# Optimization experiments

Measured on AMD Instinct MI355X. Metric: run time of the kernel, lower is better.

Reference implementation:

```python
import jax, jax.numpy as jnp
import numpy as np

# dims
N = 50000      # total nodes in merged batch graph
M = 250000     # edges for GNN propagation
E = 200000     # candidate edges scored by mixture-Bernoulli head
MAXN = 512     # max_num_nodes (padded adjacency row length)
H = 128        # hidden_dim = embedding_dim = msg_dim
EF = 128       # edge_feat_dim = 2 * att_edge_dim
ATT = 128      # att_hidden_dim
K = 20         # num_mix_component
L = 3          # num_GNN_layers
S = 512        # num_subgraph
B = 16         # batch of graphs
C = 1          # num_canonical_order


def setup_inputs() -> dict:
    key = jax.random.key(0)
    ks = list(jax.random.split(key, 64))
    it = iter(ks)
    nk = lambda: next(it)
    d = {}
    d['node_feat'] = jax.random.normal(nk(), (N, MAXN), jnp.float32)
    d['edge'] = jax.random.randint(nk(), (M, 2), 0, N, dtype=jnp.int32)
    d['edge_feat'] = jax.random.normal(nk(), (M, EF), jnp.float32)
    d['node_idx_gnn'] = jax.random.randint(nk(), (E, 2), 0, N, dtype=jnp.int32)
    d['label'] = (jax.random.uniform(nk(), (E,)) < 0.1).astype(jnp.float32)
    # even sorted partition of E candidate edges into S subgraphs (all nonempty)
    d['subgraph_idx'] = ((jnp.arange(E) * S) // E).astype(jnp.int32)
    # bc_idx = repeat_interleave(arange(B*C), subgraphs_per_graph)
    d['bc_idx'] = jnp.repeat(jnp.arange(B * C, dtype=jnp.int32), S // (B * C))
    # params
    def lin(k, out_d, in_d):
        return jax.random.normal(k, (out_d, in_d), jnp.float32) * (1.0 / np.sqrt(in_d))
    d['dec_W'] = lin(nk(), H, MAXN); d['dec_b'] = jnp.zeros((H,), jnp.float32)
    d['msg_W1'] = jnp.stack([lin(nk(), H, H + EF) for _ in range(L)])
    d['msg_b1'] = jnp.zeros((L, H), jnp.float32)
    d['msg_W2'] = jnp.stack([lin(nk(), H, H) for _ in range(L)])
    d['msg_b2'] = jnp.zeros((L, H), jnp.float32)
    d['att_W1'] = jnp.stack([lin(nk(), ATT, H + EF) for _ in range(L)])
    d['att_b1'] = jnp.zeros((L, ATT), jnp.float32)
    d['att_W2'] = jnp.stack([lin(nk(), H, ATT) for _ in range(L)])
    d['att_b2'] = jnp.zeros((L, H), jnp.float32)
    d['gru_Wih'] = jnp.stack([lin(nk(), 3 * H, H) for _ in range(L)])
    d['gru_bih'] = jnp.zeros((L, 3 * H), jnp.float32)
    d['gru_Whh'] = jnp.stack([lin(nk(), 3 * H, H) for _ in range(L)])
    d['gru_bhh'] = jnp.zeros((L, 3 * H), jnp.float32)
    d['th_W1'] = lin(nk(), H, H); d['th_b1'] = jnp.zeros((H,), jnp.float32)
    d['th_W2'] = lin(nk(), H, H); d['th_b2'] = jnp.zeros((H,), jnp.float32)
    d['th_W3'] = lin(nk(), K, H); d['th_b3'] = jnp.zeros((K,), jnp.float32)
    d['al_W1'] = lin(nk(), H, H); d['al_b1'] = jnp.zeros((H,), jnp.float32)
    d['al_W2'] = lin(nk(), H, H); d['al_b2'] = jnp.zeros((H,), jnp.float32)
    d['al_W3'] = lin(nk(), K, H); d['al_b3'] = jnp.zeros((K,), jnp.float32)
    return d


def _gran_forward(node_feat, edge_feat, label, dec_W, dec_b, msg_W1, msg_b1,
                  msg_W2, msg_b2, att_W1, att_b1, att_W2, att_b2, gru_Wih,
                  gru_bih, gru_Whh, gru_bhh, th_W1, th_b1, th_W2, th_b2,
                  th_W3, th_b3, al_W1, al_b1, al_W2, al_b2, al_W3, al_b3,
                  edge, node_idx_gnn, subgraph_idx, bc_idx):
    n = node_feat.shape[0]
    # decoder_input: Linear(max_num_nodes -> embedding_dim)
    state = node_feat @ dec_W.T + dec_b  # [N, H]
    src, dst = edge[:, 0], edge[:, 1]
    for l in range(L):
        if l > 0:
            state = jax.nn.relu(state)
        # _prop: gather diff, msg MLP, sigmoid attention gate, scatter-sum, GRU
        diff = state[src] - state[dst]                       # [M, H]
        ei = jnp.concatenate([diff, edge_feat], axis=1)      # [M, H+EF]
        msg = jax.nn.relu(ei @ msg_W1[l].T + msg_b1[l]) @ msg_W2[l].T + msg_b2[l]
        att = jax.nn.sigmoid(jax.nn.relu(ei @ att_W1[l].T + att_b1[l]) @ att_W2[l].T + att_b2[l])
        agg = jax.ops.segment_sum(msg * att, dst, num_segments=n)  # [N, H]
        # torch GRUCell
        gi = agg @ gru_Wih[l].T + gru_bih[l]
        gh = state @ gru_Whh[l].T + gru_bhh[l]
        i_r, i_z, i_n = jnp.split(gi, 3, axis=-1)
        h_r, h_z, h_n = jnp.split(gh, 3, axis=-1)
        r = jax.nn.sigmoid(i_r + h_r)
        z = jax.nn.sigmoid(i_z + h_z)
        nn_ = jnp.tanh(i_n + r * h_n)
        state = (1.0 - z) * nn_ + z * state
    # mixture-Bernoulli heads on candidate-edge node-state diffs
    d2 = state[node_idx_gnn[:, 0]] - state[node_idx_gnn[:, 1]]  # [E, H]
    def mlp3(x, W1, b1, W2, b2, W3, b3):
        h = jax.nn.relu(x @ W1.T + b1)
        h = jax.nn.relu(h @ W2.T + b2)
        return h @ W3.T + b3
    log_theta = mlp3(d2, th_W1, th_b1, th_W2, th_b2, th_W3, th_b3)  # [E, K]
    log_alpha = mlp3(d2, al_W1, al_b1, al_W2, al_b2, al_W3, al_b3)  # [E, K]
    # mixture_bernoulli_loss (pos_weight = 1.0)
    y = label[:, None]
    adj_loss = jax.nn.softplus(-log_theta) + (1.0 - y) * log_theta  # BCEWithLogits, [E, K]
    const = jax.ops.segment_sum(jnp.ones((label.shape[0],), log_theta.dtype), subgraph_idx, num_segments=S)
    reduce_adj = jax.ops.segment_sum(adj_loss, subgraph_idx, num_segments=S)     # [S, K]
    reduce_la = jax.ops.segment_sum(log_alpha, subgraph_idx, num_segments=S)
    reduce_la = jax.nn.log_softmax(reduce_la / const[:, None], axis=-1)
    log_prob = jax.scipy.special.logsumexp(-reduce_adj + reduce_la, axis=1)      # [S]
    bc_log_prob = jax.ops.segment_sum(log_prob, bc_idx, num_segments=B * C)
    bc_const = jax.ops.segment_sum(const, bc_idx, num_segments=B * C)
    bc_loss = (bc_log_prob / bc_const).reshape(B, C)
    b_loss = jax.scipy.special.logsumexp(bc_loss, axis=1)  # logsumexp over orderings
    return jnp.mean(-b_loss)


def reference(node_feat, edge, edge_feat, node_idx_gnn, label, subgraph_idx,
              bc_idx, dec_W, dec_b, msg_W1, msg_b1, msg_W2, msg_b2, att_W1,
              att_b1, att_W2, att_b2, gru_Wih, gru_bih, gru_Whh, gru_bhh,
              th_W1, th_b1, th_W2, th_b2, th_W3, th_b3, al_W1, al_b1, al_W2,
              al_b2, al_W3, al_b3):
    return _gran_forward(node_feat, edge_feat, label, dec_W, dec_b, msg_W1,
                         msg_b1, msg_W2, msg_b2, att_W1, att_b1, att_W2,
                         att_b2, gru_Wih, gru_bih, gru_Whh, gru_bhh, th_W1,
                         th_b1, th_W2, th_b2, th_W3, th_b3, al_W1, al_b1,
                         al_W2, al_b2, al_W3, al_b3, edge, node_idx_gnn,
                         subgraph_idx, bc_idx)
```

## Files before the change

kernel.cpp:

```cpp
#include <hip/hip_runtime.h>
#include <cstdint>
#include <cstddef>


typedef __bf16 bf16x8 __attribute__((ext_vector_type(8)));
typedef short  s16x8  __attribute__((ext_vector_type(8)));
typedef short  s16x4  __attribute__((ext_vector_type(4)));
typedef float  f32x4  __attribute__((ext_vector_type(4)));

__device__ inline unsigned short f2bf(float f) {
    return __builtin_bit_cast(unsigned short, (__bf16)f);
}
__device__ inline float bf2f(unsigned short b) {
    return __uint_as_float(((unsigned int)b) << 16);
}
__device__ inline unsigned int pk2(float a, float b) {
    return ((unsigned int)f2bf(b) << 16) | f2bf(a);
}
__device__ inline f32x4 MFMA(bf16x8 a, bf16x8 b, f32x4 c) {
    return __builtin_amdgcn_mfma_f32_16x16x32_bf16(a, b, c, 0, 0, 0);
}

__device__ inline bf16x8 ld_swz(const char* lds, int row, int unit) {
    return *(const bf16x8*)(lds + row * 256 + ((unit ^ (row & 7)) << 4));
}
__device__ inline void hid_write(char* HID, int h0, int erow, s16x4 s4) {
    int unit = h0 >> 3;
    *(s16x4*)(HID + erow * 256 + ((unit ^ (erow & 7)) << 4) + ((h0 & 4) << 1)) = s4;
}
__device__ inline s16x4 ld_swz4(const char* lds, int row, int c0) {
    int unit = c0 >> 3;
    return *(const s16x4*)(lds + row * 256 + ((unit ^ (row & 7)) << 4) + ((c0 & 4) << 1));
}
__device__ inline bf16x8 ldA(const short* __restrict__ Wb, int K, int row, int koff) {
    return *(const bf16x8*)(Wb + (size_t)row * K + koff);
}
__device__ inline bf16x8 ld_f32_frag(const float* __restrict__ p) {
    float4 a = *(const float4*)p, b = *(const float4*)(p + 4);
    s16x8 s;
    s[0] = f2bf(a.x); s[1] = f2bf(a.y); s[2] = f2bf(a.z); s[3] = f2bf(a.w);
    s[4] = f2bf(b.x); s[5] = f2bf(b.y); s[6] = f2bf(b.z); s[7] = f2bf(b.w);
    return __builtin_bit_cast(bf16x8, s);
}

#define NPACK 31
struct PrepackArgs {
    const float* src[NPACK];
    short*       dst[NPACK];
    int stride[NPACK];
    int rows[NPACK];
    int rowsTot[NPACK];
    int cols[NPACK];
};

__global__ void prepack(PrepackArgs a) {
    int e = blockIdx.y;
    int row = blockIdx.x;
    if (row >= a.rowsTot[e]) return;
    int c8 = threadIdx.x;
    if (c8 * 8 >= a.cols[e]) return;
    s16x8 s = {};
    if (row < a.rows[e]) {
        const float* p = a.src[e] + (size_t)row * a.stride[e] + c8 * 8;
        float4 x = *(const float4*)p, y = *(const float4*)(p + 4);
        s[0] = f2bf(x.x); s[1] = f2bf(x.y); s[2] = f2bf(x.z); s[3] = f2bf(x.w);
        s[4] = f2bf(y.x); s[5] = f2bf(y.y); s[6] = f2bf(y.z); s[7] = f2bf(y.w);
    }
    *(s16x8*)(a.dst[e] + (size_t)row * a.cols[e] + c8 * 8) = s;
}

__device__ inline void proj_gemm_store(const char* ST, char* PJ,
                                       const short* __restrict__ projW,
                                       short* __restrict__ proj,
                                       int rb, int R, int tid)
{
    const int l = tid & 63, w = tid >> 6;
    f32x4 accP[2][2][4] = {};
#pragma unroll
    for (int ks = 0; ks < 4; ++ks) {
        int koff = ks * 32 + (l >> 4) * 8;
        bf16x8 aw[2][2];
#pragma unroll
        for (int pc = 0; pc < 2; ++pc)
#pragma unroll
            for (int mt = 0; mt < 2; ++mt)
                aw[pc][mt] = ldA(projW, 128, pc * 128 + 32 * w + 16 * mt + (l & 15), koff);
#pragma unroll
        for (int n = 0; n < 4; ++n) {
            bf16x8 b = ld_swz(ST, 16 * n + (l & 15), ks * 4 + (l >> 4));
#pragma unroll
            for (int pc = 0; pc < 2; ++pc)
#pragma unroll
                for (int mt = 0; mt < 2; ++mt)
                    accP[pc][mt][n] = MFMA(aw[pc][mt], b, accP[pc][mt][n]);
        }
    }
    const int half = w >> 1;
#pragma unroll
    for (int hh = 0; hh < 2; ++hh) {
        __syncthreads();
        if (half == hh) {
#pragma unroll
            for (int pc = 0; pc < 2; ++pc)
#pragma unroll
                for (int mt = 0; mt < 2; ++mt) {
                    int h0 = 32 * w + 16 * mt + ((l >> 4) << 2);
                    int colp = 2 * h0 + 4 * pc - 128 * hh;
#pragma unroll
                    for (int n = 0; n < 4; ++n) {
                        f32x4 v = accP[pc][mt][n];
                        s16x4 s4;
                        s4[0] = f2bf(v[0]); s4[1] = f2bf(v[1]);
                        s4[2] = f2bf(v[2]); s4[3] = f2bf(v[3]);
                        hid_write(PJ, colp, 16 * n + (l & 15), s4);
                    }
                }
        }
        __syncthreads();
#pragma unroll
        for (int p2 = 0; p2 < 4; ++p2) {
            int row = p2 * 16 + (tid >> 4);
            int r = rb + row;
            if (r < R) {
                bf16x8 v = ld_swz(PJ, row, tid & 15);
                *(s16x8*)(proj + (size_t)r * 256 + hh * 128 + (tid & 15) * 8) =
                    __builtin_bit_cast(s16x8, v);
            }
        }
    }
}

__global__ __launch_bounds__(256, 3)
void dec_proj(const float* __restrict__ nf, int R,
              const short* __restrict__ decWb, const float* __restrict__ bias,
              const short* __restrict__ projW,
              short* __restrict__ sOut, short* __restrict__ proj)
{
    __shared__ char ST[16384];
    __shared__ char PJ[16384];
    const int tid = threadIdx.x, l = tid & 63, w = tid >> 6;
    const int rb = blockIdx.x * 64;

    const float* brow[4];
#pragma unroll
    for (int n = 0; n < 4; ++n) {
        int row = rb + 16 * n + (l & 15); if (row >= R) row = R - 1;
        brow[n] = nf + (size_t)row * 512;
    }

    f32x4 acc[2][4] = {};
    for (int kc = 0; kc < 512; kc += 128) {
#pragma unroll
        for (int ks = 0; ks < 4; ++ks) {
            int koff = kc + ks * 32 + (l >> 4) * 8;
            bf16x8 a0 = ldA(decWb, 512, 32 * w + (l & 15), koff);
            bf16x8 a1 = ldA(decWb, 512, 32 * w + 16 + (l & 15), koff);
#pragma unroll
            for (int n = 0; n < 4; ++n) {
                bf16x8 b = ld_f32_frag(brow[n] + koff);
                acc[0][n] = MFMA(a0, b, acc[0][n]);
                acc[1][n] = MFMA(a1, b, acc[1][n]);
            }
        }
    }
#pragma unroll
    for (int mt = 0; mt < 2; ++mt) {
        int c0 = 32 * w + 16 * mt + ((l >> 4) << 2);
        float4 bv = *(const float4*)&bias[c0];
#pragma unroll
        for (int n = 0; n < 4; ++n) {
            f32x4 v = acc[mt][n];
            s16x4 s4;
            s4[0] = f2bf(v[0] + bv.x); s4[1] = f2bf(v[1] + bv.y);
            s4[2] = f2bf(v[2] + bv.z); s4[3] = f2bf(v[3] + bv.w);
            hid_write(ST, c0, 16 * n + (l & 15), s4);
        }
    }
    __syncthreads();
#pragma unroll
    for (int p2 = 0; p2 < 4; ++p2) {
        int row = p2 * 16 + (tid >> 4);
        int r = rb + row;
        if (r < R) {
            bf16x8 v = ld_swz(ST, row, tid & 15);
            *(s16x8*)(sOut + (size_t)r * 128 + (tid & 15) * 8) =
                __builtin_bit_cast(s16x8, v);
        }
    }
    proj_gemm_store(ST, PJ, projW, proj, rb, R, tid);
}

template<int HAS_PROJ>
__global__ __launch_bounds__(256, 3)
void node_fused6(const short* __restrict__ msgatt, const int* __restrict__ rowptr,
                 const short* __restrict__ sin_,
                 const short* __restrict__ Wih, const short* __restrict__ Whh,
                 const float* __restrict__ bih, const float* __restrict__ bhh,
                 const short* __restrict__ projW,
                 short* __restrict__ sOut, short* __restrict__ proj, int R)
{
    __shared__ char AGT[16384];
    __shared__ char SIN[16384];
    __shared__ char ST[16384];
    const int tid = threadIdx.x, l = tid & 63, w = tid >> 6;
    const int rb = blockIdx.x * 64;

#pragma unroll 1
    for (int pass = 0; pass < 4; ++pass) {
        int row = pass * 16 + (tid >> 4);
        int node = rb + row;
        int u = tid & 15;
        float acc[8] = {};
        s16x8 sv = {};
        if (node < R) {
            int b = rowptr[node], e = rowptr[node + 1];
            for (int i = b; i < e; ++i) {
                s16x8 x = *(const s16x8*)(msgatt + (size_t)i * 128 + u * 8);
#pragma unroll
                for (int j = 0; j < 8; ++j) acc[j] += bf2f((unsigned short)x[j]);
            }
            sv = *(const s16x8*)(sin_ + (size_t)node * 128 + u * 8);
        }
        s16x8 o;
#pragma unroll
        for (int j = 0; j < 8; ++j) o[j] = f2bf(acc[j]);
        *(s16x8*)(AGT + row * 256 + ((u ^ (row & 7)) << 4)) = o;
        *(s16x8*)(SIN + row * 256 + ((u ^ (row & 7)) << 4)) = sv;
    }
    __syncthreads();

#pragma unroll 1
    for (int nh = 0; nh < 2; ++nh) {
        unsigned int rpk[2][2][2], zpk[2][2][2];
#pragma unroll 1
        for (int p = 0; p < 3; ++p) {
            f32x4 gia[2][2] = {}, gha[2][2] = {};
#pragma unroll
            for (int ks = 0; ks < 4; ++ks) {
                int koff = ks * 32 + (l >> 4) * 8;
                bf16x8 ai0 = ldA(Wih, 128, p * 128 + 32 * w + (l & 15), koff);
                bf16x8 ai1 = ldA(Wih, 128, p * 128 + 32 * w + 16 + (l & 15), koff);
                bf16x8 ah0 = ldA(Whh, 128, p * 128 + 32 * w + (l & 15), koff);
                bf16x8 ah1 = ldA(Whh, 128, p * 128 + 32 * w + 16 + (l & 15), koff);
#pragma unroll
                for (int n = 0; n < 2; ++n) {
                    int row = 32 * nh + 16 * n + (l & 15);
                    bf16x8 ba = ld_swz(AGT, row, ks * 4 + (l >> 4));
                    bf16x8 bs = ld_swz(SIN, row, ks * 4 + (l >> 4));
                    gia[0][n] = MFMA(ai0, ba, gia[0][n]);
                    gia[1][n] = MFMA(ai1, ba, gia[1][n]);
                    gha[0][n] = MFMA(ah0, bs, gha[0][n]);
                    gha[1][n] = MFMA(ah1, bs, gha[1][n]);
                }
            }
#pragma unroll
            for (int mt = 0; mt < 2; ++mt) {
                int c0 = 32 * w + 16 * mt + ((l >> 4) << 2);
                float4 bi = *(const float4*)&bih[p * 128 + c0];
                float4 bh = *(const float4*)&bhh[p * 128 + c0];
                float biv[4] = {bi.x, bi.y, bi.z, bi.w};
                float bhv[4] = {bh.x, bh.y, bh.z, bh.w};
#pragma unroll
                for (int n = 0; n < 2; ++n) {
                    int row = 32 * nh + 16 * n + (l & 15);
                    float gv[4], hv[4];
#pragma unroll
                    for (int q = 0; q < 4; ++q) {
                        gv[q] = gia[mt][n][q] + biv[q];
                        hv[q] = gha[mt][n][q] + bhv[q];
                    }
                    if (p == 0) {
                        rpk[mt][n][0] = pk2(1.f / (1.f + expf(-(gv[0] + hv[0]))),
                                            1.f / (1.f + expf(-(gv[1] + hv[1]))));
                        rpk[mt][n][1] = pk2(1.f / (1.f + expf(-(gv[2] + hv[2]))),
                                            1.f / (1.f + expf(-(gv[3] + hv[3]))));
                    } else if (p == 1) {
                        zpk[mt][n][0] = pk2(1.f / (1.f + expf(-(gv[0] + hv[0]))),
                                            1.f / (1.f + expf(-(gv[1] + hv[1]))));
                        zpk[mt][n][1] = pk2(1.f / (1.f + expf(-(gv[2] + hv[2]))),
                                            1.f / (1.f + expf(-(gv[3] + hv[3]))));
                    } else {
                        s16x4 sv = ld_swz4(SIN, row, c0);
                        s16x4 s4;
#pragma unroll
                        for (int q = 0; q < 4; ++q) {
                            unsigned int ru = rpk[mt][n][q >> 1], zu = zpk[mt][n][q >> 1];
                            float r = bf2f((unsigned short)((q & 1) ? (ru >> 16) : (ru & 0xffffu)));
                            float z = bf2f((unsigned short)((q & 1) ? (zu >> 16) : (zu & 0xffffu)));
                            float nn = tanhf(gv[q] + r * hv[q]);
                            float o = (1.f - z) * nn + z * bf2f((unsigned short)sv[q]);
                            s4[q] = f2bf(HAS_PROJ ? fmaxf(o, 0.f) : o);
                        }
                        hid_write(ST, c0, row, s4);
                    }
                }
            }
        }
    }
    __syncthreads();
#pragma unroll
    for (int p2 = 0; p2 < 4; ++p2) {
        int row = p2 * 16 + (tid >> 4);
        int r = rb + row;
        if (r < R) {
            bf16x8 v = ld_swz(ST, row, tid & 15);
            *(s16x8*)(sOut + (size_t)r * 128 + (tid & 15) * 8) =
                __builtin_bit_cast(s16x8, v);
        }
    }
    if (HAS_PROJ)
        proj_gemm_store(ST, AGT, projW, proj, rb, R, tid);
}

__global__ __launch_bounds__(256, 3)
void edge_fused2(const short* __restrict__ efc,
                 const int* __restrict__ srcs, const int* __restrict__ dsts,
                 const short* __restrict__ proj,
                 const short* __restrict__ mW1b, const short* __restrict__ mW2,
                 const short* __restrict__ aW1b, const short* __restrict__ aW2,
                 const float* __restrict__ mb1, const float* __restrict__ mb2,
                 const float* __restrict__ ab1, const float* __restrict__ ab2,
                 short* __restrict__ msgatt, int M, int ntiles)
{
    __shared__ char HIDm[16384];
    __shared__ char HIDa[16384];
    const int tid = threadIdx.x, l = tid & 63, w = tid >> 6;
    int q = ntiles >> 3, r = ntiles & 7;
    int xcd = blockIdx.x & 7, o = blockIdx.x >> 3;
    int tile = (xcd < r ? xcd * (q + 1) : r * (q + 1) + (xcd - r) * q) + o;
    const int pb = tile * 64;

    const char* erow[4];
    int dstv[4];
    s16x8 psv[2][4];
    {
#pragma unroll
        for (int n = 0; n < 4; ++n) {
            int pos = pb + 16 * n + (l & 15); if (pos >= M) pos = M - 1;
            int sv = srcs[pos];
            dstv[n] = dsts[pos];
            erow[n] = (const char*)(efc + (size_t)pos * 128);
#pragma unroll
            for (int mt = 0; mt < 2; ++mt) {
                int off = 2 * (32 * w + 16 * mt + ((l >> 4) << 2));
                psv[mt][n] = *(const s16x8*)(proj + (size_t)sv * 256 + off);
            }
        }
    }

    f32x4 accm[2][4] = {}, acca[2][4] = {};
#pragma unroll
    for (int ks = 0; ks < 4; ++ks) {
        int koff = ks * 32 + (l >> 4) * 8;
        bf16x8 am0 = ldA(mW1b, 128, 32 * w + (l & 15), koff);
        bf16x8 am1 = ldA(mW1b, 128, 32 * w + 16 + (l & 15), koff);
        bf16x8 aa0 = ldA(aW1b, 128, 32 * w + (l & 15), koff);
        bf16x8 aa1 = ldA(aW1b, 128, 32 * w + 16 + (l & 15), koff);
#pragma unroll
        for (int n = 0; n < 4; ++n) {
            bf16x8 b = *(const bf16x8*)(erow[n] + koff * 2);
            accm[0][n] = MFMA(am0, b, accm[0][n]);
            accm[1][n] = MFMA(am1, b, accm[1][n]);
            acca[0][n] = MFMA(aa0, b, acca[0][n]);
            acca[1][n] = MFMA(aa1, b, acca[1][n]);
        }
    }
#pragma unroll
    for (int mt = 0; mt < 2; ++mt) {
        int h0 = 32 * w + 16 * mt + ((l >> 4) << 2);
        float4 bm = *(const float4*)&mb1[h0];
        float4 ba = *(const float4*)&ab1[h0];
        float bmv[4] = {bm.x, bm.y, bm.z, bm.w};
        float bav[4] = {ba.x, ba.y, ba.z, ba.w};
#pragma unroll
        for (int n = 0; n < 4; ++n) {
            s16x8 ps = psv[mt][n];
            s16x8 pd = *(const s16x8*)(proj + (size_t)dstv[n] * 256 + 2 * h0);
            f32x4 vm = accm[mt][n], va = acca[mt][n];
            s16x4 sm, sa;
#pragma unroll
            for (int qq = 0; qq < 4; ++qq) {
                float m_ = vm[qq] + bmv[qq] + bf2f((unsigned short)ps[qq])
                           - bf2f((unsigned short)pd[qq]);
                float a_ = va[qq] + bav[qq] + bf2f((unsigned short)ps[qq + 4])
                           - bf2f((unsigned short)pd[qq + 4]);
                sm[qq] = f2bf(fmaxf(m_, 0.f));
                sa[qq] = f2bf(fmaxf(a_, 0.f));
            }
            hid_write(HIDm, h0, 16 * n + (l & 15), sm);
            hid_write(HIDa, h0, 16 * n + (l & 15), sa);
        }
    }
    __syncthreads();

    f32x4 acc2m[2][4] = {}, acc2a[2][4] = {};
#pragma unroll
    for (int ks = 0; ks < 4; ++ks) {
        int koff = ks * 32 + (l >> 4) * 8;
        bf16x8 wm0 = ldA(mW2, 128, 32 * w + (l & 15), koff);
        bf16x8 wm1 = ldA(mW2, 128, 32 * w + 16 + (l & 15), koff);
        bf16x8 wa0 = ldA(aW2, 128, 32 * w + (l & 15), koff);
        bf16x8 wa1 = ldA(aW2, 128, 32 * w + 16 + (l & 15), koff);
#pragma unroll
        for (int n = 0; n < 4; ++n) {
            bf16x8 bm = ld_swz(HIDm, 16 * n + (l & 15), ks * 4 + (l >> 4));
            bf16x8 ba = ld_swz(HIDa, 16 * n + (l & 15), ks * 4 + (l >> 4));
            acc2m[0][n] = MFMA(wm0, bm, acc2m[0][n]);
            acc2m[1][n] = MFMA(wm1, bm, acc2m[1][n]);
            acc2a[0][n] = MFMA(wa0, ba, acc2a[0][n]);
            acc2a[1][n] = MFMA(wa1, ba, acc2a[1][n]);
        }
    }
    __syncthreads();
#pragma unroll
    for (int mt = 0; mt < 2; ++mt) {
        int c0 = 32 * w + 16 * mt + ((l >> 4) << 2);
        float4 bm2 = *(const float4*)&mb2[c0];
        float4 ba2 = *(const float4*)&ab2[c0];
#pragma unroll
        for (int n = 0; n < 4; ++n) {
            f32x4 m_ = acc2m[mt][n], a_ = acc2a[mt][n];
            float o0 = (m_[0] + bm2.x) / (1.f + expf(-(a_[0] + ba2.x)));
            float o1 = (m_[1] + bm2.y) / (1.f + expf(-(a_[1] + ba2.y)));
            float o2 = (m_[2] + bm2.z) / (1.f + expf(-(a_[2] + ba2.z)));
            float o3 = (m_[3] + bm2.w) / (1.f + expf(-(a_[3] + ba2.w)));
            s16x4 s4;
            s4[0] = f2bf(o0); s4[1] = f2bf(o1); s4[2] = f2bf(o2); s4[3] = f2bf(o3);
            hid_write(HIDm, c0, 16 * n + (l & 15), s4);
        }
    }
    __syncthreads();
#pragma unroll
    for (int p2 = 0; p2 < 4; ++p2) {
        int row = p2 * 16 + (tid >> 4);
        int pos = pb + row;
        if (pos < M) {
            bf16x8 v = ld_swz(HIDm, row, tid & 15);
            *(s16x8*)(msgatt + (size_t)pos * 128 + (tid & 15) * 8) =
                __builtin_bit_cast(s16x8, v);
        }
    }
}

__global__ __launch_bounds__(256, 4)
void mlp_loss(const short* __restrict__ sP, const int* __restrict__ gidx,
              const float* __restrict__ label, const int* __restrict__ sg,
              const short* __restrict__ thW1, const short* __restrict__ thW2,
              const short* __restrict__ thW3,
              const float* __restrict__ thb1, const float* __restrict__ thb2,
              const float* __restrict__ thb3,
              const short* __restrict__ alW1, const short* __restrict__ alW2,
              const short* __restrict__ alW3,
              const float* __restrict__ alb1, const float* __restrict__ alb2,
              const float* __restrict__ alb3,
              float* __restrict__ radj, float* __restrict__ rla,
              float* __restrict__ cntS, int E, int S)
{
    __shared__ char D2T[16384];
    __shared__ char HID[16384];
    __shared__ float sacc[2][2][20];
    __shared__ float scnt[2];
    __shared__ int sbase;
    const int tid = threadIdx.x, l = tid & 63, w = tid >> 6;
    const int eb = blockIdx.x * 64;

    if (tid == 0) sbase = sg[eb];
    if (tid < 80) sacc[tid / 40][(tid / 20) & 1][tid % 20] = 0.f;

    if (w == 0) {
        int e = eb + l;
        bool valid = e < E;
        int lsv = valid ? sg[e] - sg[eb] : -1;
        unsigned long long m0 = __ballot(lsv == 0);
        unsigned long long m1 = __ballot(lsv == 1);
        if (l == 0) { scnt[0] = (float)__popcll(m0); scnt[1] = (float)__popcll(m1); }
    }

    for (int i = tid; i < 64 * 16; i += 256) {
        int row = i >> 4, u = i & 15;
        int e = eb + row; if (e >= E) e = E - 1;
        int2 ab = *(const int2*)&gidx[2 * (size_t)e];
        s16x8 x = *(const s16x8*)(sP + (size_t)ab.x * 128 + u * 8);
        s16x8 y = *(const s16x8*)(sP + (size_t)ab.y * 128 + u * 8);
        s16x8 d;
#pragma unroll
        for (int j = 0; j < 8; ++j)
            d[j] = f2bf(bf2f((unsigned short)x[j]) - bf2f((unsigned short)y[j]));
        *(s16x8*)(D2T + row * 256 + ((u ^ (row & 7)) << 4)) = d;
    }
    __syncthreads();

#pragma unroll 1
    for (int pass = 0; pass < 2; ++pass) {
        const short* W1 = pass ? alW1 : thW1;
        const short* W2 = pass ? alW2 : thW2;
        const short* W3 = pass ? alW3 : thW3;
        const float* b1 = pass ? alb1 : thb1;
        const float* b2 = pass ? alb2 : thb2;
        const float* b3 = pass ? alb3 : thb3;

        f32x4 acc[2][4] = {};
#pragma unroll
        for (int ks = 0; ks < 4; ++ks) {
            int koff = ks * 32 + (l >> 4) * 8;
            bf16x8 a0 = ldA(W1, 128, 32 * w + (l & 15), koff);
            bf16x8 a1 = ldA(W1, 128, 32 * w + 16 + (l & 15), koff);
#pragma unroll
            for (int n = 0; n < 4; ++n) {
                bf16x8 b = ld_swz(D2T, 16 * n + (l & 15), ks * 4 + (l >> 4));
                acc[0][n] = MFMA(a0, b, acc[0][n]);
                acc[1][n] = MFMA(a1, b, acc[1][n]);
            }
        }
        __syncthreads();
#pragma unroll
        for (int mt = 0; mt < 2; ++mt) {
            int h0 = 32 * w + 16 * mt + ((l >> 4) << 2);
            float4 bv = *(const float4*)&b1[h0];
#pragma unroll
            for (int n = 0; n < 4; ++n) {
                f32x4 v = acc[mt][n];
                s16x4 s4;
                s4[0] = f2bf(fmaxf(v[0] + bv.x, 0.f));
                s4[1] = f2bf(fmaxf(v[1] + bv.y, 0.f));
                s4[2] = f2bf(fmaxf(v[2] + bv.z, 0.f));
                s4[3] = f2bf(fmaxf(v[3] + bv.w, 0.f));
                hid_write(HID, h0, 16 * n + (l & 15), s4);
            }
        }
        __syncthreads();
        f32x4 acc2[2][4] = {};
#pragma unroll
        for (int ks = 0; ks < 4; ++ks) {
            int koff = ks * 32 + (l >> 4) * 8;
            bf16x8 a0 = ldA(W2, 128, 32 * w + (l & 15), koff);
            bf16x8 a1 = ldA(W2, 128, 32 * w + 16 + (l & 15), koff);
#pragma unroll
            for (int n = 0; n < 4; ++n) {
                bf16x8 b = ld_swz(HID, 16 * n + (l & 15), ks * 4 + (l >> 4));
                acc2[0][n] = MFMA(a0, b, acc2[0][n]);
                acc2[1][n] = MFMA(a1, b, acc2[1][n]);
            }
        }
        __syncthreads();
#pragma unroll
        for (int mt = 0; mt < 2; ++mt) {
            int h0 = 32 * w + 16 * mt + ((l >> 4) << 2);
            float4 bv = *(const float4*)&b2[h0];
#pragma unroll
            for (int n = 0; n < 4; ++n) {
                f32x4 v = acc2[mt][n];
                s16x4 s4;
                s4[0] = f2bf(fmaxf(v[0] + bv.x, 0.f));
                s4[1] = f2bf(fmaxf(v[1] + bv.y, 0.f));
                s4[2] = f2bf(fmaxf(v[2] + bv.z, 0.f));
                s4[3] = f2bf(fmaxf(v[3] + bv.w, 0.f));
                hid_write(HID, h0, 16 * n + (l & 15), s4);
            }
        }
        __syncthreads();
        f32x4 acc3[2] = {};
#pragma unroll
        for (int ks = 0; ks < 4; ++ks) {
            int koff = ks * 32 + (l >> 4) * 8;
            bf16x8 a0 = ldA(W3, 128, (l & 15), koff);
            bf16x8 a1 = ldA(W3, 128, 16 + (l & 15), koff);
            bf16x8 b = ld_swz(HID, 16 * w + (l & 15), ks * 4 + (l >> 4));
            acc3[0] = MFMA(a0, b, acc3[0]);
            acc3[1] = MFMA(a1, b, acc3[1]);
        }
        {
            int e = eb + 16 * w + (l & 15);
            bool val = e < E;
            float lsf = val ? (float)(sg[e] - sbase) : 0.f;
            float yv = (pass == 0 && val) ? label[e] : 0.f;
#pragma unroll
            for (int mt = 0; mt < 2; ++mt) {
#pragma unroll
                for (int qq = 0; qq < 4; ++qq) {
                    int k = 16 * mt + ((l >> 4) << 2) + qq;
                    bool kok = k < 20;
                    float bk = kok ? b3[k] : 0.f;
                    float vv = 0.f;
                    if (val && kok) {
                        float t = acc3[mt][qq] + bk;
                        if (pass == 0) {
                            float sp = fmaxf(-t, 0.f) + log1pf(expf(-fabsf(t)));
                            vv = sp + (1.f - yv) * t;
                        } else {
                            vv = t;
                        }
                    }
                    float vA = vv * (1.f - lsf), vB = vv * lsf;
                    vA += __shfl_xor(vA, 1); vB += __shfl_xor(vB, 1);
                    vA += __shfl_xor(vA, 2); vB += __shfl_xor(vB, 2);
                    vA += __shfl_xor(vA, 4); vB += __shfl_xor(vB, 4);
                    vA += __shfl_xor(vA, 8); vB += __shfl_xor(vB, 8);
                    if ((l & 15) == 0 && kok) {
                        atomicAdd(&sacc[pass][0][k], vA);
                        if (vB != 0.f) atomicAdd(&sacc[pass][1][k], vB);
                    }
                }
            }
        }
    }
    __syncthreads();
    if (tid < 40) {
        int ls = tid / 20, k = tid % 20;
        int s = sbase + ls;
        if (s < S) {
            float v  = sacc[0][ls][k];
            float v2 = sacc[1][ls][k];
            if (v  != 0.f) atomicAdd(&radj[s * 20 + k], v);
            if (v2 != 0.f) atomicAdd(&rla[s * 20 + k], v2);
        }
    }
    if (tid < 2) {
        int s = sbase + tid;
        if (s < S && scnt[tid] != 0.f) atomicAdd(&cntS[s], scnt[tid]);
    }
}

__global__ void csr_count(const int* __restrict__ edge, int* __restrict__ cnt, int M) {
    int e = blockIdx.x * 256 + threadIdx.x;
    if (e < M) atomicAdd(&cnt[edge[2 * (size_t)e + 1]], 1);
}

__global__ void csr_scan(const int* __restrict__ cnt, int* __restrict__ rowptr,
                         int* __restrict__ wofs, int N)
{
    __shared__ int part[1024];
    int t = threadIdx.x;
    int chunk = (N + 1023) / 1024;
    int b0 = t * chunk, b1 = b0 + chunk; if (b1 > N) b1 = N; if (b0 > N) b0 = N;
    int s = 0;
    for (int i = b0; i < b1; ++i) s += cnt[i];
    part[t] = s;
    __syncthreads();
    for (int off = 1; off < 1024; off <<= 1) {
        int v = (t >= off) ? part[t - off] : 0;
        __syncthreads();
        part[t] += v;
        __syncthreads();
    }
    int run = (t ? part[t - 1] : 0);
    for (int i = b0; i < b1; ++i) { rowptr[i] = run; wofs[i] = run; run += cnt[i]; }
    if (t == 1023) rowptr[N] = run;
}

__global__ void csr_scatter2(const int* __restrict__ edge, int* __restrict__ wofs,
                             int* __restrict__ eidx, int* __restrict__ srcs,
                             int* __restrict__ dsts, int M)
{
    int e = blockIdx.x * 256 + threadIdx.x;
    if (e < M) {
        int2 sd = *(const int2*)&edge[2 * (size_t)e];
        int p = atomicAdd(&wofs[sd.y], 1);
        eidx[p] = e; srcs[p] = sd.x; dsts[p] = sd.y;
    }
}

__global__ void ef_gather(const float* __restrict__ ef, const int* __restrict__ eidx,
                          short* __restrict__ efc, int M)
{
    long i = (long)blockIdx.x * 256 + threadIdx.x;
    if (i >= (long)M * 16) return;
    int p = (int)(i >> 4), u = (int)(i & 15);
    int e = eidx[p];
    const float* sp = ef + (size_t)e * 128 + u * 8;
    float4 a = *(const float4*)sp, b = *(const float4*)(sp + 4);
    s16x8 s;
    s[0] = f2bf(a.x); s[1] = f2bf(a.y); s[2] = f2bf(a.z); s[3] = f2bf(a.w);
    s[4] = f2bf(b.x); s[5] = f2bf(b.y); s[6] = f2bf(b.z); s[7] = f2bf(b.w);
    *(s16x8*)(efc + (size_t)p * 128 + u * 8) = s;
}

__global__ void final_kernel(const float* __restrict__ radj, const float* __restrict__ rla,
                             const float* __restrict__ cnt, const int* __restrict__ bc_idx,
                             float* __restrict__ out)
{
    __shared__ float bcl[16], bcc[16];
    const int s = threadIdx.x;
    if (s < 16) { bcl[s] = 0.f; bcc[s] = 0.f; }
    __syncthreads();
    float c = cnt[s];
    float x[20];
    float mx = -1e30f;
#pragma unroll
    for (int k = 0; k < 20; ++k) { x[k] = rla[s * 20 + k] / c; mx = fmaxf(mx, x[k]); }
    float se = 0.f;
#pragma unroll
    for (int k = 0; k < 20; ++k) se += expf(x[k] - mx);
    float lse = mx + logf(se);
    float t[20];
    float m2 = -1e30f;
#pragma unroll
    for (int k = 0; k < 20; ++k) { t[k] = -radj[s * 20 + k] + x[k] - lse; m2 = fmaxf(m2, t[k]); }
    float s2 = 0.f;
#pragma unroll
    for (int k = 0; k < 20; ++k) s2 += expf(t[k] - m2);
    float lp = m2 + logf(s2);
    atomicAdd(&bcl[bc_idx[s]], lp);
    atomicAdd(&bcc[bc_idx[s]], c);
    __syncthreads();
    if (s == 0) {
        float a = 0.f;
        for (int b = 0; b < 16; ++b) a += bcl[b] / bcc[b];
        out[0] = -a / 16.f;
    }
}

extern "C" void kernel_launch(void* const* d_in, const int* in_sizes, int n_in,
                              void* d_out, int out_size, void* d_ws, size_t ws_size,
                              hipStream_t stream)
{
    const float* node_feat = (const float*)d_in[0];
    const int*   edge      = (const int*)  d_in[1];
    const float* edge_feat = (const float*)d_in[2];
    const int*   gnn_idx   = (const int*)  d_in[3];
    const float* label     = (const float*)d_in[4];
    const int*   sg_idx    = (const int*)  d_in[5];
    const int*   bc_idx    = (const int*)  d_in[6];
    const float* dec_W  = (const float*)d_in[7];
    const float* dec_b  = (const float*)d_in[8];
    const float* msg_W1 = (const float*)d_in[9];
    const float* msg_b1 = (const float*)d_in[10];
    const float* msg_W2 = (const float*)d_in[11];
    const float* msg_b2 = (const float*)d_in[12];
    const float* att_W1 = (const float*)d_in[13];
    const float* att_b1 = (const float*)d_in[14];
    const float* att_W2 = (const float*)d_in[15];
    const float* att_b2 = (const float*)d_in[16];
    const float* gru_Wih = (const float*)d_in[17];
    const float* gru_bih = (const float*)d_in[18];
    const float* gru_Whh = (const float*)d_in[19];
    const float* gru_bhh = (const float*)d_in[20];
    const float* th_W1 = (const float*)d_in[21];
    const float* th_b1 = (const float*)d_in[22];
    const float* th_W2 = (const float*)d_in[23];
    const float* th_b2 = (const float*)d_in[24];
    const float* th_W3 = (const float*)d_in[25];
    const float* th_b3 = (const float*)d_in[26];
    const float* al_W1 = (const float*)d_in[27];
    const float* al_b1 = (const float*)d_in[28];
    const float* al_W2 = (const float*)d_in[29];
    const float* al_b2 = (const float*)d_in[30];
    const float* al_W3 = (const float*)d_in[31];
    const float* al_b3 = (const float*)d_in[32];

    const int N = in_sizes[0] / 512;
    const int M = in_sizes[1] / 2;
    const int E = in_sizes[3] / 2;
    const int S = in_sizes[6];

    size_t off = 0;
    auto alloc = [&](size_t bytes) {
        char* p = (char*)d_ws + off;
        off += (bytes + 255) & ~(size_t)255;
        return p;
    };
    short* decWb  = (short*)alloc((size_t)128 * 512 * 2);
    short* projWb = (short*)alloc((size_t)3 * 256 * 128 * 2);
    short* mW1bB  = (short*)alloc((size_t)3 * 128 * 128 * 2);
    short* aW1bB  = (short*)alloc((size_t)3 * 128 * 128 * 2);
    short* mW2B   = (short*)alloc((size_t)3 * 128 * 128 * 2);
    short* aW2B   = (short*)alloc((size_t)3 * 128 * 128 * 2);
    short* gihB   = (short*)alloc((size_t)3 * 384 * 128 * 2);
    short* ghhB   = (short*)alloc((size_t)3 * 384 * 128 * 2);
    short* thW1B  = (short*)alloc((size_t)128 * 128 * 2);
    short* thW2B  = (short*)alloc((size_t)128 * 128 * 2);
    short* thW3B  = (short*)alloc((size_t)32 * 128 * 2);
    short* alW1B  = (short*)alloc((size_t)128 * 128 * 2);
    short* alW2B  = (short*)alloc((size_t)128 * 128 * 2);
    short* alW3B  = (short*)alloc((size_t)32 * 128 * 2);
    short* sA     = (short*)alloc((size_t)N * 128 * 2);
    short* sB     = (short*)alloc((size_t)N * 128 * 2);
    short* sP     = (short*)alloc((size_t)N * 128 * 2);
    short* efc    = (short*)alloc((size_t)M * 128 * 2);
    short* msgatt = (short*)alloc((size_t)M * 128 * 2);
    short* proj   = (short*)alloc((size_t)N * 256 * 2);
    int*   cntN   = (int*)  alloc((size_t)N * 4);
    int*   wofs   = (int*)  alloc((size_t)N * 4);
    int*   rowptr = (int*)  alloc((size_t)(N + 1) * 4);
    int*   eidx   = (int*)  alloc((size_t)M * 4);
    int*   srcs   = (int*)  alloc((size_t)M * 4);
    int*   dsts   = (int*)  alloc((size_t)M * 4);
    float* radj   = (float*)alloc((size_t)S * 20 * 4);
    float* rla    = (float*)alloc((size_t)S * 20 * 4);
    float* cntS   = (float*)alloc((size_t)S * 4);

    PrepackArgs pa;
    int ei = 0;
    auto add = [&](const float* s, short* d, int stride, int rows, int rowsTot, int cols) {
        pa.src[ei] = s; pa.dst[ei] = d; pa.stride[ei] = stride;
        pa.rows[ei] = rows; pa.rowsTot[ei] = rowsTot; pa.cols[ei] = cols; ++ei;
    };
    add(dec_W, decWb, 512, 128, 128, 512);
    for (int l = 0; l < 3; ++l) {
        add(msg_W1 + (size_t)l * 128 * 256,       projWb + (size_t)l * 256 * 128,          256, 128, 128, 128);
        add(att_W1 + (size_t)l * 128 * 256,       projWb + (size_t)l * 256 * 128 + 16384,  256, 128, 128, 128);
        add(msg_W1 + (size_t)l * 128 * 256 + 128, mW1bB + (size_t)l * 16384,               256, 128, 128, 128);
        add(att_W1 + (size_t)l * 128 * 256 + 128, aW1bB + (size_t)l * 16384,               256, 128, 128, 128);
        add(msg_W2 + (size_t)l * 16384,           mW2B + (size_t)l * 16384,                128, 128, 128, 128);
        add(att_W2 + (size_t)l * 16384,           aW2B + (size_t)l * 16384,                128, 128, 128, 128);
        add(gru_Wih + (size_t)l * 49152,          gihB + (size_t)l * 49152,                128, 384, 384, 128);
        add(gru_Whh + (size_t)l * 49152,          ghhB + (size_t)l * 49152,                128, 384, 384, 128);
    }
    add(th_W1, thW1B, 128, 128, 128, 128);
    add(th_W2, thW2B, 128, 128, 128, 128);
    add(th_W3, thW3B, 128, 20, 32, 128);
    add(al_W1, alW1B, 128, 128, 128, 128);
    add(al_W2, alW2B, 128, 128, 128, 128);
    add(al_W3, alW3B, 128, 20, 32, 128);

    const dim3 blk(256);
    const int gN64 = (N + 63) / 64;
    const int gE64 = (E + 63) / 64;
    const int gMt  = (M + 255) / 256;
    const int ntilesM = (M + 63) / 64;

    hipMemsetAsync(radj, 0, (size_t)(S * 20 * 2 + S) * 4, stream);
    hipMemsetAsync(cntN, 0, (size_t)N * 4, stream);

    prepack<<<dim3(384, NPACK), dim3(64), 0, stream>>>(pa);

    csr_count   <<<gMt, blk, 0, stream>>>(edge, cntN, M);
    csr_scan    <<<1, 1024, 0, stream>>>(cntN, rowptr, wofs, N);
    csr_scatter2<<<gMt, blk, 0, stream>>>(edge, wofs, eidx, srcs, dsts, M);
    ef_gather   <<<(int)(((long)M * 16 + 255) / 256), blk, 0, stream>>>(edge_feat, eidx, efc, M);

    dec_proj<<<gN64, blk, 0, stream>>>(node_feat, N, decWb, dec_b, projWb, sA, proj);

    short* bufs[2] = { sA, sB };
    for (int l = 0; l < 3; ++l) {
        short* sin  = bufs[l & 1];
        short* sout = (l == 2) ? sP : bufs[(l + 1) & 1];
        edge_fused2<<<ntilesM, blk, 0, stream>>>(efc, srcs, dsts, proj,
            mW1bB + (size_t)l * 16384, mW2B + (size_t)l * 16384,
            aW1bB + (size_t)l * 16384, aW2B + (size_t)l * 16384,
            msg_b1 + l * 128, msg_b2 + l * 128,
            att_b1 + l * 128, att_b2 + l * 128,
            msgatt, M, ntilesM);
        if (l < 2) {
            node_fused6<1><<<gN64, blk, 0, stream>>>(msgatt, rowptr, sin,
                gihB + (size_t)l * 49152, ghhB + (size_t)l * 49152,
                gru_bih + l * 384, gru_bhh + l * 384,
                projWb + (size_t)(l + 1) * 256 * 128, sout, proj, N);
        } else {
            node_fused6<0><<<gN64, blk, 0, stream>>>(msgatt, rowptr, sin,
                gihB + (size_t)l * 49152, ghhB + (size_t)l * 49152,
                gru_bih + l * 384, gru_bhh + l * 384,
                nullptr, sout, nullptr, N);
        }
    }

    mlp_loss<<<gE64, blk, 0, stream>>>(sP, gnn_idx, label, sg_idx,
        thW1B, thW2B, thW3B, th_b1, th_b2, th_b3,
        alW1B, alW2B, alW3B, al_b1, al_b2, al_b3,
        radj, rla, cntS, E, S);
    final_kernel<<<1, S, 0, stream>>>(radj, rla, cntS, bc_idx, (float*)d_out);
}
```

Measured before the change: 1.063 ms.

## Compute W1 state term per edge from gathered state difference instead of node projections

Removes the per-node projection GEMM and its N×256 bf16 buffer from the decoder and node kernels. The edge kernel instead gathers source and destination state rows (128 wide), forms their difference in shared memory, and multiplies by the first-half W1 weights with MFMA. This halves the per-edge gather bytes and drops the projection stores. In exchange it adds a per-edge GEMM over M edges rather than N nodes, plus an extra shared buffer and barrier, with bf16 rounding of the difference.

```diff
diff --git a/kernel.cpp b/kernel.cpp
--- a/kernel.cpp
+++ b/kernel.cpp
@@ -69,75 +69,12 @@
     *(s16x8*)(a.dst[e] + (size_t)row * a.cols[e] + c8 * 8) = s;
 }
 
-__device__ inline void proj_gemm_store(const char* ST, char* PJ,
-                                       const short* __restrict__ projW,
-                                       short* __restrict__ proj,
-                                       int rb, int R, int tid)
-{
-    const int l = tid & 63, w = tid >> 6;
-    f32x4 accP[2][2][4] = {};
-#pragma unroll
-    for (int ks = 0; ks < 4; ++ks) {
-        int koff = ks * 32 + (l >> 4) * 8;
-        bf16x8 aw[2][2];
-#pragma unroll
-        for (int pc = 0; pc < 2; ++pc)
-#pragma unroll
-            for (int mt = 0; mt < 2; ++mt)
-                aw[pc][mt] = ldA(projW, 128, pc * 128 + 32 * w + 16 * mt + (l & 15), koff);
-#pragma unroll
-        for (int n = 0; n < 4; ++n) {
-            bf16x8 b = ld_swz(ST, 16 * n + (l & 15), ks * 4 + (l >> 4));
-#pragma unroll
-            for (int pc = 0; pc < 2; ++pc)
-#pragma unroll
-                for (int mt = 0; mt < 2; ++mt)
-                    accP[pc][mt][n] = MFMA(aw[pc][mt], b, accP[pc][mt][n]);
-        }
-    }
-    const int half = w >> 1;
-#pragma unroll
-    for (int hh = 0; hh < 2; ++hh) {
-        __syncthreads();
-        if (half == hh) {
-#pragma unroll
-            for (int pc = 0; pc < 2; ++pc)
-#pragma unroll
-                for (int mt = 0; mt < 2; ++mt) {
-                    int h0 = 32 * w + 16 * mt + ((l >> 4) << 2);
-                    int colp = 2 * h0 + 4 * pc - 128 * hh;
-#pragma unroll
-                    for (int n = 0; n < 4; ++n) {
-                        f32x4 v = accP[pc][mt][n];
-                        s16x4 s4;
-                        s4[0] = f2bf(v[0]); s4[1] = f2bf(v[1]);
-                        s4[2] = f2bf(v[2]); s4[3] = f2bf(v[3]);
-                        hid_write(PJ, colp, 16 * n + (l & 15), s4);
-                    }
-                }
-        }
-        __syncthreads();
-#pragma unroll
-        for (int p2 = 0; p2 < 4; ++p2) {
-            int row = p2 * 16 + (tid >> 4);
-            int r = rb + row;
-            if (r < R) {
-                bf16x8 v = ld_swz(PJ, row, tid & 15);
-                *(s16x8*)(proj + (size_t)r * 256 + hh * 128 + (tid & 15) * 8) =
-                    __builtin_bit_cast(s16x8, v);
-            }
-        }
-    }
-}
-
 __global__ __launch_bounds__(256, 3)
-void dec_proj(const float* __restrict__ nf, int R,
-              const short* __restrict__ decWb, const float* __restrict__ bias,
-              const short* __restrict__ projW,
-              short* __restrict__ sOut, short* __restrict__ proj)
+void dec_kernel(const float* __restrict__ nf, int R,
+                const short* __restrict__ decWb, const float* __restrict__ bias,
+                short* __restrict__ sOut)
 {
     __shared__ char ST[16384];
-    __shared__ char PJ[16384];
     const int tid = threadIdx.x, l = tid & 63, w = tid >> 6;
     const int rb = blockIdx.x * 64;
 
@@ -187,17 +124,15 @@
                 __builtin_bit_cast(s16x8, v);
         }
     }
-    proj_gemm_store(ST, PJ, projW, proj, rb, R, tid);
-}
-
-template<int HAS_PROJ>
+}
+
+template<int HAS_RELU>
 __global__ __launch_bounds__(256, 3)
-void node_fused6(const short* __restrict__ msgatt, const int* __restrict__ rowptr,
+void node_fused7(const short* __restrict__ msgatt, const int* __restrict__ rowptr,
                  const short* __restrict__ sin_,
                  const short* __restrict__ Wih, const short* __restrict__ Whh,
                  const float* __restrict__ bih, const float* __restrict__ bhh,
-                 const short* __restrict__ projW,
-                 short* __restrict__ sOut, short* __restrict__ proj, int R)
+                 short* __restrict__ sOut, int R)
 {
     __shared__ char AGT[16384];
     __shared__ char SIN[16384];
@@ -289,7 +224,7 @@
                             float z = bf2f((unsigned short)((q & 1) ? (zu >> 16) : (zu & 0xffffu)));
                             float nn = tanhf(gv[q] + r * hv[q]);
                             float o = (1.f - z) * nn + z * bf2f((unsigned short)sv[q]);
-                            s4[q] = f2bf(HAS_PROJ ? fmaxf(o, 0.f) : o);
+                            s4[q] = f2bf(HAS_RELU ? fmaxf(o, 0.f) : o);
                         }
                         hid_write(ST, c0, row, s4);
                     }
@@ -308,20 +243,21 @@
                 __builtin_bit_cast(s16x8, v);
         }
     }
-    if (HAS_PROJ)
-        proj_gemm_store(ST, AGT, projW, proj, rb, R, tid);
 }
 
 __global__ __launch_bounds__(256, 3)
-void edge_fused2(const short* __restrict__ efc,
+void edge_fused7(const short* __restrict__ efc,
                  const int* __restrict__ srcs, const int* __restrict__ dsts,
-                 const short* __restrict__ proj,
-                 const short* __restrict__ mW1b, const short* __restrict__ mW2,
-                 const short* __restrict__ aW1b, const short* __restrict__ aW2,
+                 const short* __restrict__ state,
+                 const short* __restrict__ mW1a, const short* __restrict__ mW1b,
+                 const short* __restrict__ mW2,
+                 const short* __restrict__ aW1a, const short* __restrict__ aW1b,
+                 const short* __restrict__ aW2,
                  const float* __restrict__ mb1, const float* __restrict__ mb2,
                  const float* __restrict__ ab1, const float* __restrict__ ab2,
                  short* __restrict__ msgatt, int M, int ntiles)
 {
+    __shared__ char DIF[16384];
     __shared__ char HIDm[16384];
     __shared__ char HIDa[16384];
     const int tid = threadIdx.x, l = tid & 63, w = tid >> 6;
@@ -330,25 +266,45 @@
     int tile = (xcd < r ? xcd * (q + 1) : r * (q + 1) + (xcd - r) * q) + o;
     const int pb = tile * 64;
 
+#pragma unroll 1
+    for (int i = tid; i < 64 * 16; i += 256) {
+        int row = i >> 4, u = i & 15;
+        int pos = pb + row; if (pos >= M) pos = M - 1;
+        int sv = srcs[pos], dv = dsts[pos];
+        s16x8 x = *(const s16x8*)(state + (size_t)sv * 128 + u * 8);
+        s16x8 y = *(const s16x8*)(state + (size_t)dv * 128 + u * 8);
+        s16x8 d;
+#pragma unroll
+        for (int j = 0; j < 8; ++j)
+            d[j] = f2bf(bf2f((unsigned short)x[j]) - bf2f((unsigned short)y[j]));
+        *(s16x8*)(DIF + row * 256 + ((u ^ (row & 7)) << 4)) = d;
+    }
+    __syncthreads();
+
     const char* erow[4];
-    int dstv[4];
-    s16x8 psv[2][4];
-    {
+#pragma unroll
+    for (int n = 0; n < 4; ++n) {
+        int pos = pb + 16 * n + (l & 15); if (pos >= M) pos = M - 1;
+        erow[n] = (const char*)(efc + (size_t)pos * 128);
+    }
+
+    f32x4 accm[2][4] = {}, acca[2][4] = {};
+#pragma unroll
+    for (int ks = 0; ks < 4; ++ks) {
+        int koff = ks * 32 + (l >> 4) * 8;
+        bf16x8 am0 = ldA(mW1a, 128, 32 * w + (l & 15), koff);
+        bf16x8 am1 = ldA(mW1a, 128, 32 * w + 16 + (l & 15), koff);
+        bf16x8 aa0 = ldA(aW1a, 128, 32 * w + (l & 15), koff);
+        bf16x8 aa1 = ldA(aW1a, 128, 32 * w + 16 + (l & 15), koff);
 #pragma unroll
         for (int n = 0; n < 4; ++n) {
-            int pos = pb + 16 * n + (l & 15); if (pos >= M) pos = M - 1;
-            int sv = srcs[pos];
-            dstv[n] = dsts[pos];
-            erow[n] = (const char*)(efc + (size_t)pos * 128);
-#pragma unroll
-            for (int mt = 0; mt < 2; ++mt) {
-                int off = 2 * (32 * w + 16 * mt + ((l >> 4) << 2));
-                psv[mt][n] = *(const s16x8*)(proj + (size_t)sv * 256 + off);
-            }
-        }
-    }
-
-    f32x4 accm[2][4] = {}, acca[2][4] = {};
+            bf16x8 b = ld_swz(DIF, 16 * n + (l & 15), ks * 4 + (l >> 4));
+            accm[0][n] = MFMA(am0, b, accm[0][n]);
+            accm[1][n] = MFMA(am1, b, accm[1][n]);
+            acca[0][n] = MFMA(aa0, b, acca[0][n]);
+            acca[1][n] = MFMA(aa1, b, acca[1][n]);
+        }
+    }
 #pragma unroll
     for (int ks = 0; ks < 4; ++ks) {
         int koff = ks * 32 + (l >> 4) * 8;
@@ -374,18 +330,12 @@
         float bav[4] = {ba.x, ba.y, ba.z, ba.w};
 #pragma unroll
         for (int n = 0; n < 4; ++n) {
-            s16x8 ps = psv[mt][n];
-            s16x8 pd = *(const s16x8*)(proj + (size_t)dstv[n] * 256 + 2 * h0);
             f32x4 vm = accm[mt][n], va = acca[mt][n];
             s16x4 sm, sa;
 #pragma unroll
             for (int qq = 0; qq < 4; ++qq) {
-                float m_ = vm[qq] + bmv[qq] + bf2f((unsigned short)ps[qq])
-                           - bf2f((unsigned short)pd[qq]);
-                float a_ = va[qq] + bav[qq] + bf2f((unsigned short)ps[qq + 4])
-                           - bf2f((unsigned short)pd[qq + 4]);
-                sm[qq] = f2bf(fmaxf(m_, 0.f));
-                sa[qq] = f2bf(fmaxf(a_, 0.f));
+                sm[qq] = f2bf(fmaxf(vm[qq] + bmv[qq], 0.f));
+                sa[qq] = f2bf(fmaxf(va[qq] + bav[qq], 0.f));
             }
             hid_write(HIDm, h0, 16 * n + (l & 15), sm);
             hid_write(HIDa, h0, 16 * n + (l & 15), sa);
@@ -760,7 +710,8 @@
         return p;
     };
     short* decWb  = (short*)alloc((size_t)128 * 512 * 2);
-    short* projWb = (short*)alloc((size_t)3 * 256 * 128 * 2);
+    short* mW1aB  = (short*)alloc((size_t)3 * 128 * 128 * 2);
+    short* aW1aB  = (short*)alloc((size_t)3 * 128 * 128 * 2);
     short* mW1bB  = (short*)alloc((size_t)3 * 128 * 128 * 2);
     short* aW1bB  = (short*)alloc((size_t)3 * 128 * 128 * 2);
     short* mW2B   = (short*)alloc((size_t)3 * 128 * 128 * 2);
@@ -778,7 +729,6 @@
     short* sP     = (short*)alloc((size_t)N * 128 * 2);
     short* efc    = (short*)alloc((size_t)M * 128 * 2);
     short* msgatt = (short*)alloc((size_t)M * 128 * 2);
-    short* proj   = (short*)alloc((size_t)N * 256 * 2);
     int*   cntN   = (int*)  alloc((size_t)N * 4);
     int*   wofs   = (int*)  alloc((size_t)N * 4);
     int*   rowptr = (int*)  alloc((size_t)(N + 1) * 4);
@@ -797,14 +747,14 @@
     };
     add(dec_W, decWb, 512, 128, 128, 512);
     for (int l = 0; l < 3; ++l) {
-        add(msg_W1 + (size_t)l * 128 * 256,       projWb + (size_t)l * 256 * 128,          256, 128, 128, 128);
-        add(att_W1 + (size_t)l * 128 * 256,       projWb + (size_t)l * 256 * 128 + 16384,  256, 128, 128, 128);
-        add(msg_W1 + (size_t)l * 128 * 256 + 128, mW1bB + (size_t)l * 16384,               256, 128, 128, 128);
-        add(att_W1 + (size_t)l * 128 * 256 + 128, aW1bB + (size_t)l * 16384,               256, 128, 128, 128);
-        add(msg_W2 + (size_t)l * 16384,           mW2B + (size_t)l * 16384,                128, 128, 128, 128);
-        add(att_W2 + (size_t)l * 16384,           aW2B + (size_t)l * 16384,                128, 128, 128, 128);
-        add(gru_Wih + (size_t)l * 49152,          gihB + (size_t)l * 49152,                128, 384, 384, 128);
-        add(gru_Whh + (size_t)l * 49152,          ghhB + (size_t)l * 49152,                128, 384, 384, 128);
+        add(msg_W1 + (size_t)l * 128 * 256,       mW1aB + (size_t)l * 16384, 256, 128, 128, 128);
+        add(att_W1 + (size_t)l * 128 * 256,       aW1aB + (size_t)l * 16384, 256, 128, 128, 128);
+        add(msg_W1 + (size_t)l * 128 * 256 + 128, mW1bB + (size_t)l * 16384, 256, 128, 128, 128);
+        add(att_W1 + (size_t)l * 128 * 256 + 128, aW1bB + (size_t)l * 16384, 256, 128, 128, 128);
+        add(msg_W2 + (size_t)l * 16384,           mW2B + (size_t)l * 16384,  128, 128, 128, 128);
+        add(att_W2 + (size_t)l * 16384,           aW2B + (size_t)l * 16384,  128, 128, 128, 128);
+        add(gru_Wih + (size_t)l * 49152,          gihB + (size_t)l * 49152,  128, 384, 384, 128);
+        add(gru_Whh + (size_t)l * 49152,          ghhB + (size_t)l * 49152,  128, 384, 384, 128);
     }
     add(th_W1, thW1B, 128, 128, 128, 128);
     add(th_W2, thW2B, 128, 128, 128, 128);
@@ -829,28 +779,26 @@
     csr_scatter2<<<gMt, blk, 0, stream>>>(edge, wofs, eidx, srcs, dsts, M);
     ef_gather   <<<(int)(((long)M * 16 + 255) / 256), blk, 0, stream>>>(edge_feat, eidx, efc, M);
 
-    dec_proj<<<gN64, blk, 0, stream>>>(node_feat, N, decWb, dec_b, projWb, sA, proj);
+    dec_kernel<<<gN64, blk, 0, stream>>>(node_feat, N, decWb, dec_b, sA);
 
     short* bufs[2] = { sA, sB };
     for (int l = 0; l < 3; ++l) {
         short* sin  = bufs[l & 1];
         short* sout = (l == 2) ? sP : bufs[(l + 1) & 1];
-        edge_fused2<<<ntilesM, blk, 0, stream>>>(efc, srcs, dsts, proj,
-            mW1bB + (size_t)l * 16384, mW2B + (size_t)l * 16384,
-            aW1bB + (size_t)l * 16384, aW2B + (size_t)l * 16384,
+        edge_fused7<<<ntilesM, blk, 0, stream>>>(efc, srcs, dsts, sin,
+            mW1aB + (size_t)l * 16384, mW1bB + (size_t)l * 16384, mW2B + (size_t)l * 16384,
+            aW1aB + (size_t)l * 16384, aW1bB + (size_t)l * 16384, aW2B + (size_t)l * 16384,
             msg_b1 + l * 128, msg_b2 + l * 128,
             att_b1 + l * 128, att_b2 + l * 128,
             msgatt, M, ntilesM);
         if (l < 2) {
-            node_fused6<1><<<gN64, blk, 0, stream>>>(msgatt, rowptr, sin,
+            node_fused7<1><<<gN64, blk, 0, stream>>>(msgatt, rowptr, sin,
                 gihB + (size_t)l * 49152, ghhB + (size_t)l * 49152,
-                gru_bih + l * 384, gru_bhh + l * 384,
-                projWb + (size_t)(l + 1) * 256 * 128, sout, proj, N);
+                gru_bih + l * 384, gru_bhh + l * 384, sout, N);
         } else {
-            node_fused6<0><<<gN64, blk, 0, stream>>>(msgatt, rowptr, sin,
+            node_fused7<0><<<gN64, blk, 0, stream>>>(msgatt, rowptr, sin,
                 gihB + (size_t)l * 49152, ghhB + (size_t)l * 49152,
-                gru_bih + l * 384, gru_bhh + l * 384,
-                nullptr, sout, nullptr, N);
+                gru_bih + l * 384, gru_bhh + l * 384, sout, N);
         }
     }
 
```

New measurement: 1.103 ms. 3.8% more time.
